# Performance work log

Hardware: AMD Instinct MI355X
Metric: run time of the kernel (lower is better)

The kernel has to match this reference:

```python
import jax, jax.numpy as jnp
import numpy as np

IN_CH = 512
NUM_ANCHORS = 9  # 3 scales x 3 aspect ratios


def _conv2d(x, w, b, padding):
    # x: [N,C,H,W], w: [O,I,kh,kw]
    y = jax.lax.conv_general_dilated(
        x, w, window_strides=(1, 1), padding=padding,
        dimension_numbers=("NCHW", "OIHW", "NCHW"))
    return y + b[None, :, None, None]


def setup_inputs() -> dict:
    key = jax.random.key(0)
    ks = jax.random.split(key, 7)
    B, C, H, W = 8, IN_CH, 100, 100
    # Kaiming-ish scaled init
    x = jax.random.normal(ks[0], (B, C, H, W), dtype=jnp.float32)
    w_rpn = jax.random.normal(ks[1], (C, C, 3, 3), dtype=jnp.float32) * (1.0 / np.sqrt(C * 9))
    b_rpn = jnp.zeros((C,), dtype=jnp.float32)
    w_cls = jax.random.normal(ks[2], (NUM_ANCHORS, C, 1, 1), dtype=jnp.float32) * (1.0 / np.sqrt(C))
    b_cls = jnp.zeros((NUM_ANCHORS,), dtype=jnp.float32)
    w_bbox = jax.random.normal(ks[3], (NUM_ANCHORS * 4, C, 1, 1), dtype=jnp.float32) * (1.0 / np.sqrt(C))
    b_bbox = jnp.zeros((NUM_ANCHORS * 4,), dtype=jnp.float32)
    return {"x": x, "w_rpn": w_rpn, "b_rpn": b_rpn,
            "w_cls": w_cls, "b_cls": b_cls,
            "w_bbox": w_bbox, "b_bbox": b_bbox}


def reference(x, w_rpn, b_rpn, w_cls, b_cls, w_bbox, b_bbox):
    # RPN head: 3x3 conv + ReLU, then 1x1 objectness and bbox-delta heads.
    feat = jax.nn.relu(_conv2d(x, w_rpn, b_rpn, padding=((1, 1), (1, 1))))
    cls_scores = _conv2d(feat, w_cls, b_cls, padding=((0, 0), (0, 0)))      # [B, 9, H, W]
    bbox_deltas = _conv2d(feat, w_bbox, b_bbox, padding=((0, 0), (0, 0)))   # [B, 36, H, W]
    return cls_scores, bbox_deltas
```

## Files before the change

### kernel.cpp

```cpp
#include <hip/hip_runtime.h>
#include <stdint.h>

typedef unsigned short u16;
typedef __bf16 bf16x8 __attribute__((ext_vector_type(8)));
typedef float f32x4 __attribute__((ext_vector_type(4)));

#define XT_STRIDE 10752
#define XT_GUARD  128
#define NPAD      10496
#define NT        82

__device__ __forceinline__ float b2f(u16 u) {
  union { unsigned int i; float f; } v; v.i = ((unsigned int)u) << 16; return v.f;
}
__device__ __forceinline__ u16 f2b(float f) {
  union { float f; unsigned int i; } v; v.f = f;
  unsigned int u = v.i;
  unsigned int r = u + 0x7FFFu + ((u >> 16) & 1u);
  return (u16)(r >> 16);
}
__device__ __forceinline__ float ldin(const void* p, long i, int f32) {
  return f32 ? ((const float*)p)[i] : b2f(((const u16*)p)[i]);
}
__device__ __forceinline__ void async16(const void* g, void* l) {
  __builtin_amdgcn_global_load_lds(
      (const __attribute__((address_space(1))) unsigned int*)g,
      (__attribute__((address_space(3))) unsigned int*)l, 16, 0, 0);
}
__device__ __forceinline__ int sniff_is_f32(const void* x) {
  const uint4* p = (const uint4*)x;
  const int lane = threadIdx.x & 63;
  unsigned int acc = 0;
  #pragma unroll
  for (int i = 0; i < 16; ++i) {
    uint4 v = p[i * 64 + lane];
    unsigned int w0 = v.x, w1 = v.y, w2 = v.z, w3 = v.w;
    acc |= ((w0 & 0x7F80u) == 0x7F80u) | (((w0 >> 16) & 0x7F80u) == 0x7F80u);
    acc |= ((w1 & 0x7F80u) == 0x7F80u) | (((w1 >> 16) & 0x7F80u) == 0x7F80u);
    acc |= ((w2 & 0x7F80u) == 0x7F80u) | (((w2 >> 16) & 0x7F80u) == 0x7F80u);
    acc |= ((w3 & 0x7F80u) == 0x7F80u) | (((w3 >> 16) & 0x7F80u) == 0x7F80u);
  }
  return __any(acc != 0) ? 1 : 0;
}

__global__ __launch_bounds__(256) void k_prep(const void* __restrict__ x,
                                              const void* __restrict__ w_rpn,
                                              const void* __restrict__ b_rpn,
                                              const void* __restrict__ w_cls,
                                              const void* __restrict__ b_cls,
                                              const void* __restrict__ w_bbox,
                                              const void* __restrict__ b_bbox,
                                              u16* __restrict__ xt,
                                              u16* __restrict__ wA,
                                              u16* __restrict__ wH,
                                              float* __restrict__ bAll,
                                              int* __restrict__ flagOut) {
  const int blk = blockIdx.x;
  const int t = threadIdx.x;
  if (blk < 6400) {
    const int f32 = sniff_is_f32(x);
    if (t >= 200) return;
    const int b = blk / 800, r = blk - b * 800;
    const int h = r >> 3, cb = r & 7;
    const int co = t / 25, jw = t % 25;
    const int c0 = cb * 64 + co * 8;
    u16 v[8][4];
    if (!f32) {
      const u16* src = (const u16*)x + (long)(b * 512 + c0) * 10000 + h * 100 + jw * 4;
      #pragma unroll
      for (int dc = 0; dc < 8; ++dc) {
        uint2 u = *(const uint2*)(src + (long)dc * 10000);
        const u16* pv = (const u16*)&u;
        v[dc][0] = pv[0]; v[dc][1] = pv[1]; v[dc][2] = pv[2]; v[dc][3] = pv[3];
      }
    } else {
      const float* src = (const float*)x + (long)(b * 512 + c0) * 10000 + h * 100 + jw * 4;
      #pragma unroll
      for (int dc = 0; dc < 8; ++dc) {
        float4 u = *(const float4*)(src + (long)dc * 10000);
        v[dc][0] = f2b(u.x); v[dc][1] = f2b(u.y); v[dc][2] = f2b(u.z); v[dc][3] = f2b(u.w);
      }
    }
    u16* dst = xt + ((long)b * XT_STRIDE + XT_GUARD + (h + 1) * 102 + 1 + jw * 4) * 512 + c0;
    #pragma unroll
    for (int dw = 0; dw < 4; ++dw) {
      union { uint4 u; u16 s[8]; } pk;
      #pragma unroll
      for (int dc = 0; dc < 8; ++dc) pk.s[dc] = v[dc][dw];
      *(uint4*)(dst + (long)dw * 512) = pk.u;
    }
  } else if (blk < 7904) {
    const int i2 = blk - 6400;
    const int b = i2 / 188, bx = i2 - b * 188;
    const int i = bx * 256 + t;
    if (i >= 48128) return;
    int row, sub;
    if (i < 35328) {
      int rr = i >> 6; sub = i & 63;
      row = (rr < 230) ? rr : (10200 + rr);
    } else {
      int j = i - 35328;
      int ci = j >> 6; sub = j & 63;
      int pr = (ci >> 1) + 1;
      row = XT_GUARD + pr * 102 + (ci & 1) * 101;
    }
    uint4 z = {0, 0, 0, 0};
    *(uint4*)(xt + ((long)b * XT_STRIDE + row) * 512 + sub * 8) = z;
  } else if (blk < 8928) {
    const int f32 = sniff_is_f32(x);
    const int idx = (blk - 7904) * 256 + t;
    const int o = idx >> 9, c = idx & 511;
    u16* dst = wA + (long)o * 4608 + (c >> 6) * 576 + (c & 63);
    #pragma unroll
    for (int s = 0; s < 9; ++s) dst[s * 64] = f2b(ldin(w_rpn, (long)idx * 9 + s, f32));
  } else {
    const int f32 = sniff_is_f32(x);
    const int idx = (blk - 8928) * 256 + t;
    const int a = idx >> 9, c = idx & 511;
    float v = 0.f;
    if (a < 9) v = ldin(w_cls, a * 512 + c, f32);
    else if (a < 45) v = ldin(w_bbox, (a - 9) * 512 + c, f32);
    wH[idx] = f2b(v);
    if (idx < 512) bAll[idx] = ldin(b_rpn, idx, f32);
    if (c == 0) {
      float bv = 0.f;
      if (a < 9) bv = ldin(b_cls, a, f32);
      else if (a < 45) bv = ldin(b_bbox, a - 9, f32);
      bAll[512 + a] = bv;
    }
    if (blk == 8928 && t == 0) *flagOut = f32;
  }
}

__global__ __launch_bounds__(256, 4) void k_conv(const u16* __restrict__ xt, const u16* __restrict__ wA,
                                                 const float* __restrict__ bAll, u16* __restrict__ feat) {
  __shared__ u16 sA[128 * 64];
  __shared__ u16 sB[128 * 64];
  __shared__ float sBias[128];
  const int t = threadIdx.x;
  const int i = blockIdx.x;
  const int xcd = i & 7, j = i >> 3;
  const int mtb = j / 82, nt = j - mtb * 82;
  const int pair = xcd + 8 * mtb;
  const int mt = pair & 3, b = pair >> 2;
  const int m0 = mt * 128, n0 = nt * 128;
  if (t < 128) sBias[t] = bAll[m0 + t];
  f32x4 acc[4][4] = {};
  const int lane = t & 63, wv = t >> 6;
  const int srow = t >> 3;
  const int sseg = (((t & 7) ^ (srow & 7))) * 8;
  const int mh = (wv & 1) * 64, nh = (wv >> 1) * 64;
  const int l15 = lane & 15, q = lane >> 4;
  const int s7 = l15 & 7;
  u16* sAw = sA + wv * 512;
  u16* sBw = sB + wv * 512;
  const u16* gA = wA + (long)(m0 + srow) * 4608 + sseg;
  const u16* xtb = xt + ((long)b * XT_STRIDE + XT_GUARD) * 512;
  const u16* rowA = sA + (mh + l15) * 64;
  const u16* rowB = sB + (nh + l15) * 64;
  for (int ks = 0; ks < 72; ++ks) {
    const int k0 = ks * 64;
    const int cchunk = ks / 9;
    const int s = ks - cchunk * 9;
    const int c0 = cchunk * 64;
    const int off = (s / 3) * 102 + (s - (s / 3) * 3) - 103;
    const u16* gB = xtb + (long)(n0 + srow + off) * 512 + c0 + sseg;
    async16(gA + k0, sAw);
    async16(gA + k0 + (long)32 * 4608, sAw + 32 * 64);
    async16(gA + k0 + (long)64 * 4608, sAw + 64 * 64);
    async16(gA + k0 + (long)96 * 4608, sAw + 96 * 64);
    async16(gB,             sBw);
    async16(gB + 32 * 512,  sBw + 32 * 64);
    async16(gB + 64 * 512,  sBw + 64 * 64);
    async16(gB + 96 * 512,  sBw + 96 * 64);
    asm volatile("s_waitcnt vmcnt(0)" ::: "memory");
    __syncthreads();
    #pragma unroll
    for (int h = 0; h < 2; ++h) {
      const int segA = ((h * 4 + q) ^ s7) * 8;
      bf16x8 af[4], bf[4];
      #pragma unroll
      for (int mi = 0; mi < 4; ++mi) af[mi] = *(const bf16x8*)(rowA + mi * 1024 + segA);
      #pragma unroll
      for (int ni = 0; ni < 4; ++ni) bf[ni] = *(const bf16x8*)(rowB + ni * 1024 + segA);
      #pragma unroll
      for (int mi = 0; mi < 4; ++mi)
        #pragma unroll
        for (int ni = 0; ni < 4; ++ni)
          acc[mi][ni] = __builtin_amdgcn_mfma_f32_16x16x32_bf16(af[mi], bf[ni], acc[mi][ni], 0, 0, 0);
    }
    __syncthreads();
  }
  u16* fb = feat + (long)b * NPAD * 512;
  #pragma unroll
  for (int mi = 0; mi < 4; ++mi) {
    const int ol = mh + mi * 16 + q * 4;
    #pragma unroll
    for (int ni = 0; ni < 4; ++ni) {
      const int p = n0 + nh + ni * 16 + l15;
      unsigned long long pk = 0;
      #pragma unroll
      for (int r = 0; r < 4; ++r) {
        float v = acc[mi][ni][r] + sBias[ol + r];
        v = v > 0.f ? v : 0.f;
        pk |= ((unsigned long long)f2b(v)) << (16 * r);
      }
      *(unsigned long long*)(fb + (long)p * 512 + m0 + ol) = pk;
    }
  }
}

__global__ __launch_bounds__(256) void k_head(const u16* __restrict__ feat, const u16* __restrict__ wH,
                                              const float* __restrict__ bAll, void* __restrict__ out,
                                              const int* __restrict__ flag) {
  const int f32 = *flag;
  const int t = threadIdx.x;
  const int lane = t & 63, wv = t >> 6;
  const int l15 = lane & 15, q = lane >> 4;
  const int slot = blockIdx.x * 64 + wv * 16;
  const int b = slot / NPAD, p0 = slot - b * NPAD;
  const u16* fp = feat + ((long)b * NPAD + p0 + l15) * 512 + q * 8;
  const u16* ap = wH + (long)l15 * 512 + q * 8;
  f32x4 acc[3] = {};
  #pragma unroll
  for (int ks = 0; ks < 16; ++ks) {
    const int k0 = ks * 32;
    bf16x8 bf = *(const bf16x8*)(fp + k0);
    bf16x8 a0 = *(const bf16x8*)(ap + k0);
    bf16x8 a1 = *(const bf16x8*)(ap + 16 * 512 + k0);
    bf16x8 a2 = *(const bf16x8*)(ap + 32 * 512 + k0);
    acc[0] = __builtin_amdgcn_mfma_f32_16x16x32_bf16(a0, bf, acc[0], 0, 0, 0);
    acc[1] = __builtin_amdgcn_mfma_f32_16x16x32_bf16(a1, bf, acc[1], 0, 0, 0);
    acc[2] = __builtin_amdgcn_mfma_f32_16x16x32_bf16(a2, bf, acc[2], 0, 0, 0);
  }
  const int p = p0 + l15;
  const int pr = p / 102, pc = p - pr * 102;
  if (pr < 1 || pr > 100 || pc < 1 || pc > 100) return;
  const int h = pr - 1, w = pc - 1;
  #pragma unroll
  for (int mi = 0; mi < 3; ++mi) {
    #pragma unroll
    for (int r = 0; r < 4; ++r) {
      const int a = mi * 16 + q * 4 + r;
      if (a >= 45) continue;
      float v = acc[mi][r] + bAll[512 + a];
      long oidx;
      if (a < 9) oidx = ((long)(b * 9 + a)) * 10000 + h * 100 + w;
      else       oidx = 720000 + ((long)(b * 36 + (a - 9))) * 10000 + h * 100 + w;
      if (f32) ((float*)out)[oidx] = v;
      else     ((u16*)out)[oidx] = f2b(v);
    }
  }
}

extern "C" void kernel_launch(void* const* d_in, const int* in_sizes, int n_in,
                              void* d_out, int out_size, void* d_ws, size_t ws_size,
                              hipStream_t stream) {
  const void* x      = d_in[0];
  const void* w_rpn  = d_in[1];
  const void* b_rpn  = d_in[2];
  const void* w_cls  = d_in[3];
  const void* b_cls  = d_in[4];
  const void* w_bbox = d_in[5];
  const void* b_bbox = d_in[6];
  char* ws = (char*)d_ws;
  u16*  xt   = (u16*) (ws);
  u16*  feat = (u16*) (ws + 88080384);
  u16*  wA   = (u16*) (ws + 174063616);
  u16*  wH   = (u16*) (ws + 178782208);
  float* bAll= (float*)(ws + 178831360);
  int*  flag = (int*) (ws + 178833600);

  k_prep<<<9024, 256, 0, stream>>>(x, w_rpn, b_rpn, w_cls, b_cls, w_bbox, b_bbox,
                                   xt, wA, wH, bAll, flag);
  k_conv<<<2624, 256, 0, stream>>>(xt, wA, bAll, feat);
  k_head<<<1312, 256, 0, stream>>>(feat, wH, bAll, d_out, flag);
}
```

Measured before the change: 669.1 us.

## Rewrite implicit-GEMM conv as 256x256 tile with double-buffered 8-wave LDS pipeline

```diff
diff --git a/kernel.cpp b/kernel.cpp
--- a/kernel.cpp
+++ b/kernel.cpp
@@ -8,7 +8,6 @@
 #define XT_STRIDE 10752
 #define XT_GUARD  128
 #define NPAD      10496
-#define NT        82
 
 __device__ __forceinline__ float b2f(u16 u) {
   union { unsigned int i; float f; } v; v.i = ((unsigned int)u) << 16; return v.f;
@@ -132,76 +131,189 @@
   }
 }
 
-__global__ __launch_bounds__(256, 4) void k_conv(const u16* __restrict__ xt, const u16* __restrict__ wA,
+#define BARX() do { asm volatile("" ::: "memory"); __builtin_amdgcn_s_barrier(); asm volatile("" ::: "memory"); } while (0)
+#define MF(d, a_, b_) d = __builtin_amdgcn_mfma_f32_16x16x32_bf16(a_, b_, d, 0, 0, 0)
+
+__global__ __launch_bounds__(512, 2) void k_conv(const u16* __restrict__ xt, const u16* __restrict__ wA,
                                                  const float* __restrict__ bAll, u16* __restrict__ feat) {
-  __shared__ u16 sA[128 * 64];
-  __shared__ u16 sB[128 * 64];
-  __shared__ float sBias[128];
+  __shared__ u16 lds[65536];
   const int t = threadIdx.x;
   const int i = blockIdx.x;
-  const int xcd = i & 7, j = i >> 3;
-  const int mtb = j / 82, nt = j - mtb * 82;
-  const int pair = xcd + 8 * mtb;
-  const int mt = pair & 3, b = pair >> 2;
-  const int m0 = mt * 128, n0 = nt * 128;
-  if (t < 128) sBias[t] = bAll[m0 + t];
-  f32x4 acc[4][4] = {};
+  const int b = i & 7;
+  const int j = i >> 3;
+  const int nt = j >> 1, mt = j & 1;
+  const int m0 = mt * 256, n0 = nt * 256;
   const int lane = t & 63, wv = t >> 6;
+  const int wr = wv >> 2, wn = wv & 3;
+  const int l15 = lane & 15, q = lane >> 4, s7 = l15 & 7;
   const int srow = t >> 3;
-  const int sseg = (((t & 7) ^ (srow & 7))) * 8;
-  const int mh = (wv & 1) * 64, nh = (wv >> 1) * 64;
-  const int l15 = lane & 15, q = lane >> 4;
-  const int s7 = l15 & 7;
-  u16* sAw = sA + wv * 512;
-  u16* sBw = sB + wv * 512;
+  const int sseg = ((t & 7) ^ (srow & 7)) * 8;
   const u16* gA = wA + (long)(m0 + srow) * 4608 + sseg;
-  const u16* xtb = xt + ((long)b * XT_STRIDE + XT_GUARD) * 512;
-  const u16* rowA = sA + (mh + l15) * 64;
-  const u16* rowB = sB + (nh + l15) * 64;
-  for (int ks = 0; ks < 72; ++ks) {
-    const int k0 = ks * 64;
-    const int cchunk = ks / 9;
-    const int s = ks - cchunk * 9;
-    const int c0 = cchunk * 64;
-    const int off = (s / 3) * 102 + (s - (s / 3) * 3) - 103;
-    const u16* gB = xtb + (long)(n0 + srow + off) * 512 + c0 + sseg;
-    async16(gA + k0, sAw);
-    async16(gA + k0 + (long)32 * 4608, sAw + 32 * 64);
-    async16(gA + k0 + (long)64 * 4608, sAw + 64 * 64);
-    async16(gA + k0 + (long)96 * 4608, sAw + 96 * 64);
-    async16(gB,             sBw);
-    async16(gB + 32 * 512,  sBw + 32 * 64);
-    async16(gB + 64 * 512,  sBw + 64 * 64);
-    async16(gB + 96 * 512,  sBw + 96 * 64);
-    asm volatile("s_waitcnt vmcnt(0)" ::: "memory");
-    __syncthreads();
-    #pragma unroll
-    for (int h = 0; h < 2; ++h) {
-      const int segA = ((h * 4 + q) ^ s7) * 8;
-      bf16x8 af[4], bf[4];
-      #pragma unroll
-      for (int mi = 0; mi < 4; ++mi) af[mi] = *(const bf16x8*)(rowA + mi * 1024 + segA);
-      #pragma unroll
-      for (int ni = 0; ni < 4; ++ni) bf[ni] = *(const bf16x8*)(rowB + ni * 1024 + segA);
-      #pragma unroll
-      for (int mi = 0; mi < 4; ++mi)
-        #pragma unroll
-        for (int ni = 0; ni < 4; ++ni)
-          acc[mi][ni] = __builtin_amdgcn_mfma_f32_16x16x32_bf16(af[mi], bf[ni], acc[mi][ni], 0, 0, 0);
-    }
-    __syncthreads();
-  }
+  const u16* gB = xt + ((long)b * XT_STRIDE + XT_GUARD + n0 + srow) * 512 + sseg;
+  u16* ldsw = lds + wv * 512;
+  const int rbA = (wr * 128 + l15) * 64;
+  const int rbB = 16384 + (wn * 64 + l15) * 64;
+  const int sk0 = (q ^ s7) * 8;
+  const int sk1 = ((4 + q) ^ s7) * 8;
+
+  auto stage = [&](int kt, int ln) {
+    if (kt >= 72) return;
+    const int p = kt & 1;
+    const int cchunk = kt / 9, s = kt - cchunk * 9;
+    if (ln < 4) {
+      async16(gA + (long)ln * 64 * 4608 + cchunk * 576 + s * 64,
+              ldsw + p * 32768 + ln * 4096);
+    } else {
+      const int off = (s / 3) * 102 + (s - (s / 3) * 3) - 103;
+      async16(gB + ((long)(ln - 4) * 64 + off) * 512 + cchunk * 64,
+              ldsw + p * 32768 + 16384 + (ln - 4) * 4096);
+    }
+  };
+
+  f32x4 acc[8][4] = {};
+  bf16x8 a0[4][2], a1[4][2], bb[4][2];
+
+  #pragma unroll
+  for (int ln = 0; ln < 8; ++ln) stage(0, ln);
+  #pragma unroll
+  for (int ln = 0; ln < 4; ++ln) stage(1, ln);
+  asm volatile("s_waitcnt vmcnt(4)" ::: "memory");
+  __builtin_amdgcn_s_barrier();
+
+  for (int kt = 0; kt < 72; kt += 2) {
+    const u16* L0 = lds;
+    const u16* L1 = lds + 32768;
+    #pragma unroll
+    for (int mi = 0; mi < 4; ++mi) {
+      a0[mi][0] = *(const bf16x8*)(L0 + rbA + mi * 1024 + sk0);
+      a0[mi][1] = *(const bf16x8*)(L0 + rbA + mi * 1024 + sk1);
+    }
+    #pragma unroll
+    for (int ni = 0; ni < 2; ++ni) {
+      bb[ni][0] = *(const bf16x8*)(L0 + rbB + ni * 1024 + sk0);
+      bb[ni][1] = *(const bf16x8*)(L0 + rbB + ni * 1024 + sk1);
+    }
+    stage(kt + 1, 4); stage(kt + 1, 5);
+    BARX();
+    __builtin_amdgcn_s_setprio(1);
+    #pragma unroll
+    for (int mi = 0; mi < 4; ++mi)
+      #pragma unroll
+      for (int ni = 0; ni < 2; ++ni) { MF(acc[mi][ni], a0[mi][0], bb[ni][0]); MF(acc[mi][ni], a0[mi][1], bb[ni][1]); }
+    __builtin_amdgcn_s_setprio(0);
+    BARX();
+    #pragma unroll
+    for (int mi = 0; mi < 4; ++mi) {
+      a1[mi][0] = *(const bf16x8*)(L0 + rbA + (4 + mi) * 1024 + sk0);
+      a1[mi][1] = *(const bf16x8*)(L0 + rbA + (4 + mi) * 1024 + sk1);
+    }
+    #pragma unroll
+    for (int ni = 0; ni < 2; ++ni) {
+      bb[2 + ni][0] = *(const bf16x8*)(L0 + rbB + (2 + ni) * 1024 + sk0);
+      bb[2 + ni][1] = *(const bf16x8*)(L0 + rbB + (2 + ni) * 1024 + sk1);
+    }
+    stage(kt + 1, 6); stage(kt + 1, 7);
+    BARX();
+    __builtin_amdgcn_s_setprio(1);
+    #pragma unroll
+    for (int mi = 0; mi < 4; ++mi)
+      #pragma unroll
+      for (int ni = 0; ni < 2; ++ni) { MF(acc[4 + mi][ni], a1[mi][0], bb[ni][0]); MF(acc[4 + mi][ni], a1[mi][1], bb[ni][1]); }
+    __builtin_amdgcn_s_setprio(0);
+    BARX();
+    stage(kt + 2, 0); stage(kt + 2, 1);
+    BARX();
+    __builtin_amdgcn_s_setprio(1);
+    #pragma unroll
+    for (int mi = 0; mi < 4; ++mi)
+      #pragma unroll
+      for (int ni = 0; ni < 2; ++ni) { MF(acc[mi][2 + ni], a0[mi][0], bb[2 + ni][0]); MF(acc[mi][2 + ni], a0[mi][1], bb[2 + ni][1]); }
+    __builtin_amdgcn_s_setprio(0);
+    BARX();
+    stage(kt + 2, 2); stage(kt + 2, 3);
+    BARX();
+    __builtin_amdgcn_s_setprio(1);
+    #pragma unroll
+    for (int mi = 0; mi < 4; ++mi)
+      #pragma unroll
+      for (int ni = 0; ni < 2; ++ni) { MF(acc[4 + mi][2 + ni], a1[mi][0], bb[2 + ni][0]); MF(acc[4 + mi][2 + ni], a1[mi][1], bb[2 + ni][1]); }
+    __builtin_amdgcn_s_setprio(0);
+    if (kt + 2 < 72) { asm volatile("s_waitcnt vmcnt(4)" ::: "memory"); }
+    else             { asm volatile("s_waitcnt vmcnt(0)" ::: "memory"); }
+    BARX();
+    #pragma unroll
+    for (int mi = 0; mi < 4; ++mi) {
+      a0[mi][0] = *(const bf16x8*)(L1 + rbA + mi * 1024 + sk0);
+      a0[mi][1] = *(const bf16x8*)(L1 + rbA + mi * 1024 + sk1);
+    }
+    #pragma unroll
+    for (int ni = 0; ni < 2; ++ni) {
+      bb[ni][0] = *(const bf16x8*)(L1 + rbB + ni * 1024 + sk0);
+      bb[ni][1] = *(const bf16x8*)(L1 + rbB + ni * 1024 + sk1);
+    }
+    stage(kt + 2, 4); stage(kt + 2, 5);
+    BARX();
+    __builtin_amdgcn_s_setprio(1);
+    #pragma unroll
+    for (int mi = 0; mi < 4; ++mi)
+      #pragma unroll
+      for (int ni = 0; ni < 2; ++ni) { MF(acc[mi][ni], a0[mi][0], bb[ni][0]); MF(acc[mi][ni], a0[mi][1], bb[ni][1]); }
+    __builtin_amdgcn_s_setprio(0);
+    BARX();
+    #pragma unroll
+    for (int mi = 0; mi < 4; ++mi) {
+      a1[mi][0] = *(const bf16x8*)(L1 + rbA + (4 + mi) * 1024 + sk0);
+      a1[mi][1] = *(const bf16x8*)(L1 + rbA + (4 + mi) * 1024 + sk1);
+    }
+    #pragma unroll
+    for (int ni = 0; ni < 2; ++ni) {
+      bb[2 + ni][0] = *(const bf16x8*)(L1 + rbB + (2 + ni) * 1024 + sk0);
+      bb[2 + ni][1] = *(const bf16x8*)(L1 + rbB + (2 + ni) * 1024 + sk1);
+    }
+    stage(kt + 2, 6); stage(kt + 2, 7);
+    BARX();
+    __builtin_amdgcn_s_setprio(1);
+    #pragma unroll
+    for (int mi = 0; mi < 4; ++mi)
+      #pragma unroll
+      for (int ni = 0; ni < 2; ++ni) { MF(acc[4 + mi][ni], a1[mi][0], bb[ni][0]); MF(acc[4 + mi][ni], a1[mi][1], bb[ni][1]); }
+    __builtin_amdgcn_s_setprio(0);
+    BARX();
+    stage(kt + 3, 0); stage(kt + 3, 1);
+    BARX();
+    __builtin_amdgcn_s_setprio(1);
+    #pragma unroll
+    for (int mi = 0; mi < 4; ++mi)
+      #pragma unroll
+      for (int ni = 0; ni < 2; ++ni) { MF(acc[mi][2 + ni], a0[mi][0], bb[2 + ni][0]); MF(acc[mi][2 + ni], a0[mi][1], bb[2 + ni][1]); }
+    __builtin_amdgcn_s_setprio(0);
+    BARX();
+    stage(kt + 3, 2); stage(kt + 3, 3);
+    BARX();
+    __builtin_amdgcn_s_setprio(1);
+    #pragma unroll
+    for (int mi = 0; mi < 4; ++mi)
+      #pragma unroll
+      for (int ni = 0; ni < 2; ++ni) { MF(acc[4 + mi][2 + ni], a1[mi][0], bb[2 + ni][0]); MF(acc[4 + mi][2 + ni], a1[mi][1], bb[2 + ni][1]); }
+    __builtin_amdgcn_s_setprio(0);
+    if (kt + 3 < 72) { asm volatile("s_waitcnt vmcnt(4)" ::: "memory"); }
+    else             { asm volatile("s_waitcnt vmcnt(0)" ::: "memory"); }
+    BARX();
+  }
+
   u16* fb = feat + (long)b * NPAD * 512;
   #pragma unroll
-  for (int mi = 0; mi < 4; ++mi) {
-    const int ol = mh + mi * 16 + q * 4;
+  for (int mi = 0; mi < 8; ++mi) {
+    const int ol = wr * 128 + mi * 16 + q * 4;
+    const float4 bv = *(const float4*)(bAll + m0 + ol);
+    const float bvr[4] = {bv.x, bv.y, bv.z, bv.w};
     #pragma unroll
     for (int ni = 0; ni < 4; ++ni) {
-      const int p = n0 + nh + ni * 16 + l15;
+      const int p = n0 + wn * 64 + ni * 16 + l15;
       unsigned long long pk = 0;
       #pragma unroll
       for (int r = 0; r < 4; ++r) {
-        float v = acc[mi][ni][r] + sBias[ol + r];
+        float v = acc[mi][ni][r] + bvr[r];
         v = v > 0.f ? v : 0.f;
         pk |= ((unsigned long long)f2b(v)) << (16 * r);
       }
@@ -273,6 +385,6 @@
 
   k_prep<<<9024, 256, 0, stream>>>(x, w_rpn, b_rpn, w_cls, b_cls, w_bbox, b_bbox,
                                    xt, wA, wH, bAll, flag);
-  k_conv<<<2624, 256, 0, stream>>>(xt, wA, bAll, feat);
+  k_conv<<<656, 512, 0, stream>>>(xt, wA, bAll, feat);
   k_head<<<1312, 256, 0, stream>>>(feat, wH, bAll, d_out, flag);
 }
```

Result: slower. 705.8 us (+5.5%).

## Switch conv GEMM to 32x32x16 MFMA with two-wave 128-thread blocks

Applied to the files above, without the earlier changes.

```diff
diff --git a/kernel.cpp b/kernel.cpp
--- a/kernel.cpp
+++ b/kernel.cpp
@@ -4,6 +4,7 @@
 typedef unsigned short u16;
 typedef __bf16 bf16x8 __attribute__((ext_vector_type(8)));
 typedef float f32x4 __attribute__((ext_vector_type(4)));
+typedef float f32x16 __attribute__((ext_vector_type(16)));
 
 #define XT_STRIDE 10752
 #define XT_GUARD  128
@@ -132,7 +133,7 @@
   }
 }
 
-__global__ __launch_bounds__(256, 4) void k_conv(const u16* __restrict__ xt, const u16* __restrict__ wA,
+__global__ __launch_bounds__(128, 2) void k_conv(const u16* __restrict__ xt, const u16* __restrict__ wA,
                                                  const float* __restrict__ bAll, u16* __restrict__ feat) {
   __shared__ u16 sA[128 * 64];
   __shared__ u16 sB[128 * 64];
@@ -144,20 +145,19 @@
   const int pair = xcd + 8 * mtb;
   const int mt = pair & 3, b = pair >> 2;
   const int m0 = mt * 128, n0 = nt * 128;
-  if (t < 128) sBias[t] = bAll[m0 + t];
-  f32x4 acc[4][4] = {};
+  sBias[t] = bAll[m0 + t];
+  f32x16 acc[4][2] = {};
   const int lane = t & 63, wv = t >> 6;
+  const int l31 = lane & 31, hi = lane >> 5;
+  const int s7r = l31 & 7;
   const int srow = t >> 3;
-  const int sseg = (((t & 7) ^ (srow & 7))) * 8;
-  const int mh = (wv & 1) * 64, nh = (wv >> 1) * 64;
-  const int l15 = lane & 15, q = lane >> 4;
-  const int s7 = l15 & 7;
+  const int sseg = ((t & 7) ^ (srow & 7)) * 8;
+  const u16* gA = wA + (long)(m0 + srow) * 4608 + sseg;
+  const u16* xtb = xt + ((long)b * XT_STRIDE + XT_GUARD) * 512;
   u16* sAw = sA + wv * 512;
   u16* sBw = sB + wv * 512;
-  const u16* gA = wA + (long)(m0 + srow) * 4608 + sseg;
-  const u16* xtb = xt + ((long)b * XT_STRIDE + XT_GUARD) * 512;
-  const u16* rowA = sA + (mh + l15) * 64;
-  const u16* rowB = sB + (nh + l15) * 64;
+  const u16* rowA = sA + l31 * 64;
+  const u16* rowB = sB + (wv * 64 + l31) * 64;
   for (int ks = 0; ks < 72; ++ks) {
     const int k0 = ks * 64;
     const int cchunk = ks / 9;
@@ -165,47 +165,48 @@
     const int c0 = cchunk * 64;
     const int off = (s / 3) * 102 + (s - (s / 3) * 3) - 103;
     const u16* gB = xtb + (long)(n0 + srow + off) * 512 + c0 + sseg;
-    async16(gA + k0, sAw);
-    async16(gA + k0 + (long)32 * 4608, sAw + 32 * 64);
-    async16(gA + k0 + (long)64 * 4608, sAw + 64 * 64);
-    async16(gA + k0 + (long)96 * 4608, sAw + 96 * 64);
-    async16(gB,             sBw);
-    async16(gB + 32 * 512,  sBw + 32 * 64);
-    async16(gB + 64 * 512,  sBw + 64 * 64);
-    async16(gB + 96 * 512,  sBw + 96 * 64);
+    #pragma unroll
+    for (int ci = 0; ci < 8; ++ci)
+      async16(gA + k0 + (long)ci * 16 * 4608, sAw + ci * 1024);
+    #pragma unroll
+    for (int ci = 0; ci < 8; ++ci)
+      async16(gB + (long)ci * 16 * 512, sBw + ci * 1024);
     asm volatile("s_waitcnt vmcnt(0)" ::: "memory");
     __syncthreads();
     #pragma unroll
-    for (int h = 0; h < 2; ++h) {
-      const int segA = ((h * 4 + q) ^ s7) * 8;
-      bf16x8 af[4], bf[4];
-      #pragma unroll
-      for (int mi = 0; mi < 4; ++mi) af[mi] = *(const bf16x8*)(rowA + mi * 1024 + segA);
-      #pragma unroll
-      for (int ni = 0; ni < 4; ++ni) bf[ni] = *(const bf16x8*)(rowB + ni * 1024 + segA);
+    for (int k2 = 0; k2 < 4; ++k2) {
+      const int seg = ((2 * k2 + hi) ^ s7r) * 8;
+      bf16x8 af[4], bf[2];
+      #pragma unroll
+      for (int mi = 0; mi < 4; ++mi) af[mi] = *(const bf16x8*)(rowA + mi * 2048 + seg);
+      #pragma unroll
+      for (int ni = 0; ni < 2; ++ni) bf[ni] = *(const bf16x8*)(rowB + ni * 2048 + seg);
       #pragma unroll
       for (int mi = 0; mi < 4; ++mi)
         #pragma unroll
-        for (int ni = 0; ni < 4; ++ni)
-          acc[mi][ni] = __builtin_amdgcn_mfma_f32_16x16x32_bf16(af[mi], bf[ni], acc[mi][ni], 0, 0, 0);
+        for (int ni = 0; ni < 2; ++ni)
+          acc[mi][ni] = __builtin_amdgcn_mfma_f32_32x32x16_bf16(af[mi], bf[ni], acc[mi][ni], 0, 0, 0);
     }
     __syncthreads();
   }
   u16* fb = feat + (long)b * NPAD * 512;
   #pragma unroll
   for (int mi = 0; mi < 4; ++mi) {
-    const int ol = mh + mi * 16 + q * 4;
-    #pragma unroll
-    for (int ni = 0; ni < 4; ++ni) {
-      const int p = n0 + nh + ni * 16 + l15;
-      unsigned long long pk = 0;
-      #pragma unroll
-      for (int r = 0; r < 4; ++r) {
-        float v = acc[mi][ni][r] + sBias[ol + r];
-        v = v > 0.f ? v : 0.f;
-        pk |= ((unsigned long long)f2b(v)) << (16 * r);
+    #pragma unroll
+    for (int ni = 0; ni < 2; ++ni) {
+      const int p = n0 + wv * 64 + ni * 32 + l31;
+      #pragma unroll
+      for (int qd = 0; qd < 4; ++qd) {
+        const int ob = mi * 32 + qd * 8 + hi * 4;
+        unsigned long long pk = 0;
+        #pragma unroll
+        for (int r = 0; r < 4; ++r) {
+          float v = acc[mi][ni][qd * 4 + r] + sBias[ob + r];
+          v = v > 0.f ? v : 0.f;
+          pk |= ((unsigned long long)f2b(v)) << (16 * r);
+        }
+        *(unsigned long long*)(fb + (long)p * 512 + m0 + ob) = pk;
       }
-      *(unsigned long long*)(fb + (long)p * 512 + m0 + ol) = pk;
     }
   }
 }
@@ -273,6 +274,6 @@
 
   k_prep<<<9024, 256, 0, stream>>>(x, w_rpn, b_rpn, w_cls, b_cls, w_bbox, b_bbox,
                                    xt, wA, wH, bAll, flag);
-  k_conv<<<2624, 256, 0, stream>>>(xt, wA, bAll, feat);
+  k_conv<<<2624, 128, 0, stream>>>(xt, wA, bAll, feat);
   k_head<<<1312, 256, 0, stream>>>(feat, wH, bAll, d_out, flag);
 }
```

After: 739.9 us. 10.6% more time.
